# Kernel tuning notes

Measured on AMD Instinct MI355X. Metric: run time of the kernel, lower is better.

The kernel has to match this reference:

```python
import jax, jax.numpy as jnp
import numpy as np

T, B = 32, 64
D_IN = 512      # input_size == embedding dim
H = 512         # hidden_size
V = 32000       # n_vocab
F_FEAT = 768    # feature_size
NH = 8          # num_heads
HD = H // NH    # head_dim


def setup_inputs() -> dict:
    key = jax.random.key(0)
    ks = jax.random.split(key, 16)
    s = 0.02
    inp = {
        'y': jax.random.randint(ks[0], (T, B), 0, V),
        'ctx': jax.random.normal(ks[1], (1, B, F_FEAT), jnp.float32),
        'emb_W': jax.random.normal(ks[2], (V, D_IN), jnp.float32) * s,
        # GRUCell dec0: gates ordered (r, z, n) as in torch
        'W_ih': jax.random.normal(ks[3], (3 * H, D_IN), jnp.float32) * s,
        'b_ih': jnp.zeros((3 * H,), jnp.float32),
        'W_hh': jax.random.normal(ks[4], (3 * H, H), jnp.float32) * s,
        'b_hh': jnp.zeros((3 * H,), jnp.float32),
        # FF att: feature_size -> hidden, tanh
        'W_att': jax.random.normal(ks[5], (H, F_FEAT), jnp.float32) * s,
        'b_att': jnp.zeros((H,), jnp.float32),
        # MultiHeadSelfAttention projections (hidden -> hidden)
        'Wq': jax.random.normal(ks[6], (H, H), jnp.float32) * s,
        'bq': jnp.zeros((H,), jnp.float32),
        'Wk': jax.random.normal(ks[7], (H, H), jnp.float32) * s,
        'bk': jnp.zeros((H,), jnp.float32),
        'Wv': jax.random.normal(ks[8], (H, H), jnp.float32) * s,
        'bv': jnp.zeros((H,), jnp.float32),
        'Wfc': jax.random.normal(ks[9], (H, H), jnp.float32) * s,
        'bfc': jnp.zeros((H,), jnp.float32),
        # FF hid2out: hidden -> input, tanh, bias_zero
        'W_h2o': jax.random.normal(ks[10], (D_IN, H), jnp.float32) * s,
        'b_h2o': jnp.zeros((D_IN,), jnp.float32),
        # FF out2prob: input -> vocab, linear
        'W_out': jax.random.normal(ks[11], (V, D_IN), jnp.float32) * s,
        'b_out': jnp.zeros((V,), jnp.float32),
    }
    return inp


def reference(y, ctx, emb_W, W_ih, b_ih, W_hh, b_hh, W_att, b_att,
              Wq, bq, Wk, bk, Wv, bv, Wfc, bfc, W_h2o, b_h2o, W_out, b_out):
    y_emb = emb_W[y]                                   # [T, B, D_IN]
    # ct is constant across decode steps: tanh FF over pooled image feature
    ct = jnp.tanh(ctx[0] @ W_att.T + b_att)            # [B, H]
    h0 = jnp.zeros((y.shape[1], H), y_emb.dtype)       # dec_init 'zero'

    def step(h, y_t):
        # torch GRUCell (gate order r, z, n)
        gi = y_t @ W_ih.T + b_ih                       # [B, 3H]
        gh = h @ W_hh.T + b_hh                         # [B, 3H]
        gi_r, gi_z, gi_n = jnp.split(gi, 3, axis=-1)
        gh_r, gh_z, gh_n = jnp.split(gh, 3, axis=-1)
        r = jax.nn.sigmoid(gi_r + gh_r)
        z = jax.nn.sigmoid(gi_z + gh_z)
        n = jnp.tanh(gi_n + r * gh_n)
        h1 = (1.0 - z) * n + z * h                     # [B, H]

        x = h1 * ct                                    # [B, H]
        # MultiHeadSelfAttention on a single vector, heads act as sequence
        q = (x @ Wq.T + bq).reshape(-1, NH, HD)        # [B, NH, HD]
        k = (x @ Wk.T + bk).reshape(-1, NH, HD)
        v = (x @ Wv.T + bv).reshape(-1, NH, HD)
        scores = jnp.einsum('bhd,bgd->bhg', q, k) / HD  # note: /head_dim (not sqrt)
        attw = jax.nn.softmax(scores, axis=-1)
        att_out = jnp.einsum('bhg,bgd->bhd', attw, v).reshape(-1, H)
        h2 = att_out @ Wfc.T + bfc                     # [B, H] (fc_out, vocab_size==H)

        logit = jnp.tanh(h2 @ W_h2o.T + b_h2o)         # [B, D_IN]
        prob = jax.nn.softmax(logit @ W_out.T + b_out, axis=-1)  # [B, V]
        return h1, prob                                # f_next returns h1 as next state

    _, probs = jax.lax.scan(step, h0, y_emb)           # [T, B, V]
    return probs
```

## Files before the change

### kernel.cpp

```cpp
#include <hip/hip_runtime.h>
#include <hip/hip_bf16.h>
#include <math.h>

typedef __bf16 bf16_t;
typedef __bf16 bf16x8 __attribute__((ext_vector_type(8)));
typedef __bf16 bf16x4 __attribute__((ext_vector_type(4)));
typedef float  f32x4  __attribute__((ext_vector_type(4)));

#define T_STEPS 32
#define BATCH   64
#define DIN     512
#define HID     512
#define VOCAB   32000
#define FFEAT   768
#define ROWS    2048
#define G3      1536
#define NBLK_A  32

#define EPI_F32  0
#define EPI_BF16 1
#define EPI_TANH 2

#define GLOAD16(gp, lp) __builtin_amdgcn_global_load_lds( \
    (const __attribute__((address_space(1))) void*)(gp),  \
    (__attribute__((address_space(3))) void*)(lp), 16, 0, 0)

#define PHASEK(BUF, MH, KS, STAGE_STMT, GATE_STMT)                            \
  {                                                                           \
    bf16x8 af_[4], bf_[4];                                                    \
    _Pragma("unroll")                                                         \
    for (int m2 = 0; m2 < 4; ++m2) {                                          \
      const int row = wm * 64 + m2 * 16 + la;                                 \
      const int sl = ((KS) * 4 + lg) ^ (row & 7);                             \
      af_[m2] =                                                               \
          *(const bf16x8*)&lds[((BUF)*4 + (MH)) * 8192 + row * 64 + sl * 8];  \
    }                                                                         \
    _Pragma("unroll")                                                         \
    for (int nj = 0; nj < 4; ++nj) {                                          \
      const int row = wn * 32 + (nj & 1) * 16 + la;                           \
      const int sl = ((KS) * 4 + lg) ^ (row & 7);                             \
      bf_[nj] =                                                               \
          *(const bf16x8*)&lds[((BUF)*4 + 2 + (nj >> 1)) * 8192 + row * 64 + sl * 8];\
    }                                                                         \
    STAGE_STMT;                                                               \
    GATE_STMT;                                                                \
    __builtin_amdgcn_s_barrier();                                             \
    __builtin_amdgcn_s_setprio(1);                                            \
    _Pragma("unroll")                                                         \
    for (int m2 = 0; m2 < 4; ++m2)                                            \
      _Pragma("unroll")                                                       \
      for (int nj = 0; nj < 4; ++nj)                                          \
        acc[(MH)*4 + m2][nj] =                                                \
            __builtin_amdgcn_mfma_f32_16x16x32_bf16(                          \
                af_[m2], bf_[nj], acc[(MH)*4 + m2][nj], 0, 0, 0);             \
    __builtin_amdgcn_s_setprio(0);                                            \
    __builtin_amdgcn_s_barrier();                                             \
  }

template<int KD>
__global__ __launch_bounds__(512, 2) void gemm_v(
    const bf16_t* __restrict__ A, const bf16_t* __restrict__ B,
    const float* __restrict__ bias, bf16_t* __restrict__ ecache,
    float* __restrict__ partial, int M, int N, int NB)
{
  __shared__ bf16_t lds[2 * 4 * 8192];
  __shared__ float psum[256][4];
  const int tid = threadIdx.x;
  const int lane = tid & 63, wv = tid >> 6;
  const int wm = wv >> 2, wn = wv & 3;
  const int la = lane & 15, lg = lane >> 4;

  const int lin = blockIdx.x;
  const int mt = M >> 8;
  const int cpx = (NB * mt) >> 3;
  const int wg = (lin & 7) * cpx + (lin >> 3);
  const int bn = wg / mt, bm = wg - bn * mt;

  auto stageA = [&](int buf, int h, int kt) {
    const size_t base = (size_t)(bm * 256 + h * 128) * KD + (size_t)kt * 64;
#pragma unroll
    for (int q = 0; q < 2; ++q) {
      const int L = q * 512 + tid;
      const int row = L >> 3, sl = L & 7;
      const int c = sl ^ (row & 7);
      GLOAD16(A + base + (size_t)row * KD + c * 8,
              &lds[(buf * 4 + h) * 8192 + L * 8]);
    }
  };
  auto stageB = [&](int buf, int h, int kt) {
    const size_t base = (size_t)(bn * 256 + h * 128) * KD + (size_t)kt * 64;
#pragma unroll
    for (int q = 0; q < 2; ++q) {
      const int L = q * 512 + tid;
      const int row = L >> 3, sl = L & 7;
      const int c = sl ^ (row & 7);
      GLOAD16(B + base + (size_t)row * KD + c * 8,
              &lds[(buf * 4 + 2 + h) * 8192 + L * 8]);
    }
  };

  f32x4 acc[8][4] = {};
  constexpr int NITER = KD >> 7;

  stageA(0, 0, 0); stageA(0, 1, 0); stageB(0, 0, 0); stageB(0, 1, 0);
  stageA(1, 0, 1);
  asm volatile("s_waitcnt vmcnt(2)" ::: "memory");
  __builtin_amdgcn_s_barrier();

#pragma unroll
  for (int it = 0; it < NITER; ++it) {
    const int t0 = 2 * it;
    const bool lastI = (it == NITER - 1);
    PHASEK(0, 0, 0, { stageA(1, 1, t0 + 1); stageB(1, 0, t0 + 1); }, ;)
    PHASEK(0, 0, 1, { stageB(1, 1, t0 + 1); }, ;)
    PHASEK(0, 1, 0, { if (!lastI) stageA(0, 0, t0 + 2); }, ;)
    PHASEK(0, 1, 1, { },
           { if (lastI) { asm volatile("s_waitcnt vmcnt(0)" ::: "memory"); }
             else       { asm volatile("s_waitcnt vmcnt(2)" ::: "memory"); } })
    PHASEK(1, 0, 0, { if (!lastI) { stageA(0, 1, t0 + 2); stageB(0, 0, t0 + 2); } }, ;)
    PHASEK(1, 0, 1, { if (!lastI) stageB(0, 1, t0 + 2); }, ;)
    PHASEK(1, 1, 0, { if (!lastI) stageA(1, 0, t0 + 3); }, ;)
    PHASEK(1, 1, 1, { },
           { if (!lastI) { asm volatile("s_waitcnt vmcnt(2)" ::: "memory"); } })
  }

  float bv[4];
#pragma unroll
  for (int nj = 0; nj < 4; ++nj) {
    const int col = bn * 256 + (nj >> 1) * 128 + wn * 32 + (nj & 1) * 16 + la;
    bv[nj] = bias[col];
  }
  const int odd = la & 1;
#pragma unroll
  for (int mi = 0; mi < 8; ++mi) {
#pragma unroll
    for (int rr = 0; rr < 4; ++rr) {
      const int rowl = (mi >> 2) * 128 + wm * 64 + (mi & 3) * 16 + lg * 4 + rr;
      const int row = bm * 256 + rowl;
      float vsum = 0.f;
#pragma unroll
      for (int nj = 0; nj < 4; ++nj) {
        const float e = expf(acc[mi][nj][rr] + bv[nj]);
        vsum += e;
        const unsigned int mine =
            (unsigned int)__builtin_bit_cast(unsigned short, (bf16_t)e);
        const unsigned int other = (unsigned int)__shfl_xor((int)mine, 1);
        if (!odd) {
          const int col = bn * 256 + (nj >> 1) * 128 + wn * 32 + (nj & 1) * 16 + la;
          *(unsigned int*)&ecache[(size_t)row * N + col] = mine | (other << 16);
        }
      }
      vsum += __shfl_xor(vsum, 1);
      vsum += __shfl_xor(vsum, 2);
      vsum += __shfl_xor(vsum, 4);
      vsum += __shfl_xor(vsum, 8);
      if (la == 0) psum[rowl][wn] = vsum;
    }
  }
  __syncthreads();
  if (tid < 256) {
    partial[(size_t)(bm * 256 + tid) * NB + bn] =
        psum[tid][0] + psum[tid][1] + psum[tid][2] + psum[tid][3];
  }
}

template<int EPI, int KD>
__global__ __launch_bounds__(256) void gemm_lds(
    const bf16_t* __restrict__ A, const bf16_t* __restrict__ B,
    const float* __restrict__ bias, void* __restrict__ out, int M, int N)
{
  __shared__ bf16_t As[3][128 * 32];
  __shared__ bf16_t Bs[3][128 * 32];

  const int lane = threadIdx.x & 63;
  const int wv   = threadIdx.x >> 6;
  const int wm = wv >> 1, wn = wv & 1;
  const int bn = blockIdx.x, bm = blockIdx.y;
  const int la = lane & 15, lg = lane >> 4;
  const int tid = threadIdx.x;

  auto stage = [&](int buf, int k0) {
#pragma unroll
    for (int q = 0; q < 2; ++q) {
      const int idx = q * 256 + tid;
      const int row = idx >> 2, c = idx & 3;
      const int gch = c ^ ((row >> 1) & 3);
      GLOAD16(A + (size_t)(bm * 128 + row) * KD + k0 + gch * 8, &As[buf][idx * 8]);
      GLOAD16(B + (size_t)(bn * 128 + row) * KD + k0 + gch * 8, &Bs[buf][idx * 8]);
    }
  };
  const int rdch = (lg ^ ((la >> 1) & 3)) * 8;

  f32x4 acc[4][4] = {};
  constexpr int NT = KD >> 5;
  stage(0, 0);
  stage(1, 32);
  for (int kt = 0; kt < NT; ++kt) {
    if (kt + 1 < NT) {
      asm volatile("s_waitcnt vmcnt(4)" ::: "memory");
    } else {
      asm volatile("s_waitcnt vmcnt(0)" ::: "memory");
    }
    __builtin_amdgcn_s_barrier();
    __builtin_amdgcn_sched_barrier(0);
    if (kt + 2 < NT) stage((kt + 2) % 3, (kt + 2) * 32);
    const bf16_t* Ab = As[kt % 3];
    const bf16_t* Bb = Bs[kt % 3];
    bf16x8 a[4], b[4];
#pragma unroll
    for (int i = 0; i < 4; ++i)
      a[i] = *(const bf16x8*)(Ab + (wm * 64 + i * 16 + la) * 32 + rdch);
#pragma unroll
    for (int j = 0; j < 4; ++j)
      b[j] = *(const bf16x8*)(Bb + (wn * 64 + j * 16 + la) * 32 + rdch);
    __builtin_amdgcn_s_setprio(1);
#pragma unroll
    for (int i = 0; i < 4; ++i)
#pragma unroll
      for (int j = 0; j < 4; ++j)
        acc[i][j] = __builtin_amdgcn_mfma_f32_16x16x32_bf16(a[i], b[j], acc[i][j], 0, 0, 0);
    __builtin_amdgcn_s_setprio(0);
  }

  const int m0 = bm * 128 + wm * 64;
  const int n0 = bn * 128 + wn * 64;
  float bv4[4];
#pragma unroll
  for (int j = 0; j < 4; ++j) bv4[j] = bias[n0 + j * 16 + la];
#pragma unroll
  for (int i = 0; i < 4; ++i) {
#pragma unroll
    for (int r = 0; r < 4; ++r) {
      const int row = m0 + i * 16 + lg * 4 + r;
#pragma unroll
      for (int j = 0; j < 4; ++j) {
        const int col = n0 + j * 16 + la;
        float v = acc[i][j][r] + bv4[j];
        if constexpr (EPI == EPI_F32) {
          ((float*)out)[(size_t)row * N + col] = v;
        } else if constexpr (EPI == EPI_BF16) {
          ((bf16_t*)out)[(size_t)row * N + col] = (bf16_t)v;
        } else {
          ((bf16_t*)out)[(size_t)row * N + col] = (bf16_t)tanhf(v);
        }
      }
    }
  }
}

__global__ __launch_bounds__(256) void phaseA_k(
    const bf16_t* __restrict__ Wg, const float* __restrict__ bhh,
    const float* __restrict__ gi, const float* __restrict__ ct,
    unsigned int* __restrict__ hbuf, bf16_t* __restrict__ Xall,
    int* __restrict__ flags, const float* __restrict__ Wout_f32,
    bf16_t* __restrict__ WoutB)
{
  __shared__ bf16_t Wl[48 * 520];
  __shared__ float bl[48];
  const int tid = threadIdx.x, blk = blockIdx.x;

  if (blk >= NBLK_A) {
    const int NCB = gridDim.x - NBLK_A;
    const int n4 = VOCAB * DIN / 4;
    for (int i = (blk - NBLK_A) * 256 + tid; i < n4; i += NCB * 256) {
      float4 v = ((const float4*)Wout_f32)[i];
      bf16x4 o = {(bf16_t)v.x, (bf16_t)v.y, (bf16_t)v.z, (bf16_t)v.w};
      *(bf16x4*)(WoutB + (size_t)i * 4) = o;
    }
    return;
  }

  for (int i = tid; i < 48 * 64; i += 256) {
    const int rw = i >> 6, ch = (i & 63) << 3;
    *(bf16x8*)(Wl + rw * 520 + ch) = *(const bf16x8*)(Wg + (size_t)(blk * 48 + rw) * 512 + ch);
  }
  if (tid < 48) bl[tid] = bhh[blk * 48 + tid];
  __syncthreads();

  const int lane = tid & 63, wv = tid >> 6;
  const int la = lane & 15, lg = lane >> 4;
  const int jcol = blk * 16 + la;
  const int rowA = wv * 16 + la;

  const float blr = bl[la], blz = bl[16 + la], bln = bl[32 + la];
  float hprev[4], ctv[4];
#pragma unroll
  for (int r = 0; r < 4; ++r) {
    hprev[r] = 0.f;
    ctv[r] = ct[(size_t)(wv * 16 + lg * 4 + r) * HID + jcol];
  }

  for (int t = 0; t < T_STEPS; ++t) {
    const float* girow = gi + (size_t)t * BATCH * G3 + (size_t)blk * 48;
    float gv[12];
#pragma unroll
    for (int r = 0; r < 4; ++r) {
      const float* gp = girow + (size_t)(wv * 16 + lg * 4 + r) * G3;
      gv[r * 3 + 0] = gp[la];
      gv[r * 3 + 1] = gp[16 + la];
      gv[r * 3 + 2] = gp[32 + la];
    }
    if (t > 0) {
      if (lane < 32) {
        while (__hip_atomic_load(&flags[(lane * 4 + wv) * 16], __ATOMIC_RELAXED,
                                 __HIP_MEMORY_SCOPE_AGENT) < t) { }
      }
      asm volatile("" ::: "memory");
    }
    const unsigned long long* hb =
        (const unsigned long long*)(hbuf + (size_t)(t & 1) * 16384);
    bf16x8 af[16];
#pragma unroll
    for (int q = 0; q < 16; ++q) {
      union { unsigned long long u[2]; bf16x8 v; } c;
      const size_t bidx = (size_t)(2 * q + (lg >> 1)) * 256 + rowA * 4 + (lg & 1) * 2;
      c.u[0] = __hip_atomic_load(hb + bidx,     __ATOMIC_RELAXED, __HIP_MEMORY_SCOPE_AGENT);
      c.u[1] = __hip_atomic_load(hb + bidx + 1, __ATOMIC_RELAXED, __HIP_MEMORY_SCOPE_AGENT);
      af[q] = c.v;
    }
    f32x4 acc0 = {}, acc1 = {}, acc2 = {};
#pragma unroll
    for (int q = 0; q < 16; ++q) {
      const bf16_t* wp = Wl + q * 32 + lg * 8;
      bf16x8 b0 = *(const bf16x8*)(wp + (0 * 16 + la) * 520);
      bf16x8 b1 = *(const bf16x8*)(wp + (1 * 16 + la) * 520);
      bf16x8 b2 = *(const bf16x8*)(wp + (2 * 16 + la) * 520);
      acc0 = __builtin_amdgcn_mfma_f32_16x16x32_bf16(af[q], b0, acc0, 0, 0, 0);
      acc1 = __builtin_amdgcn_mfma_f32_16x16x32_bf16(af[q], b1, acc1, 0, 0, 0);
      acc2 = __builtin_amdgcn_mfma_f32_16x16x32_bf16(af[q], b2, acc2, 0, 0, 0);
    }
    float h1v[4];
#pragma unroll
    for (int r = 0; r < 4; ++r) {
      const float ghr = acc0[r] + blr;
      const float ghz = acc1[r] + blz;
      const float ghn = acc2[r] + bln;
      const float rr = 1.f / (1.f + expf(-(gv[r * 3 + 0] + ghr)));
      const float zz = 1.f / (1.f + expf(-(gv[r * 3 + 1] + ghz)));
      const float nn = tanhf(gv[r * 3 + 2] + rr * ghn);
      h1v[r] = (1.f - zz) * nn + zz * hprev[r];
      hprev[r] = h1v[r];
    }
    unsigned int* hn = hbuf + (size_t)((t + 1) & 1) * 16384 + blk * 512;
#pragma unroll
    for (int r = 0; r < 4; ++r) {
      const int row = wv * 16 + lg * 4 + r;
      const unsigned int mine =
          (unsigned int)__builtin_bit_cast(unsigned short, (bf16_t)h1v[r]);
      const unsigned int other = (unsigned int)__shfl_xor((int)mine, 1);
      if ((la & 1) == 0) {
        __hip_atomic_store(hn + row * 8 + (la >> 1), mine | (other << 16),
                           __ATOMIC_RELAXED, __HIP_MEMORY_SCOPE_AGENT);
      }
    }
    asm volatile("s_waitcnt vmcnt(0)" ::: "memory");
    if (lane == 0) {
      __hip_atomic_store(&flags[(blk * 4 + wv) * 16], t + 1, __ATOMIC_RELAXED,
                         __HIP_MEMORY_SCOPE_AGENT);
    }
#pragma unroll
    for (int r = 0; r < 4; ++r) {
      const int row = wv * 16 + lg * 4 + r;
      Xall[((size_t)t * BATCH + row) * HID + jcol] = (bf16_t)(h1v[r] * ctv[r]);
    }
  }
}

__global__ __launch_bounds__(256) void attn_k(const bf16_t* __restrict__ QKV,
                                              bf16_t* __restrict__ attO)
{
  __shared__ float sq[4][512], sk[4][512], sv[4][512], sw[4][64];
  const int tid = threadIdx.x;
  const int wv = tid >> 6, lane = tid & 63;
  const int row = blockIdx.x * 4 + wv;
  const bf16_t* base = QKV + (size_t)row * G3;
  bf16x8 vq = *(const bf16x8*)(base + lane * 8);
  bf16x8 vk = *(const bf16x8*)(base + 512 + lane * 8);
  bf16x8 vv = *(const bf16x8*)(base + 1024 + lane * 8);
#pragma unroll
  for (int e = 0; e < 8; ++e) {
    sq[wv][lane * 8 + e] = (float)vq[e];
    sk[wv][lane * 8 + e] = (float)vk[e];
    sv[wv][lane * 8 + e] = (float)vv[e];
  }
  __syncthreads();
  const int h = lane >> 3, g = lane & 7;
  float s = 0.f;
#pragma unroll 16
  for (int d = 0; d < 64; ++d) s += sq[wv][h * 64 + d] * sk[wv][g * 64 + d];
  s *= (1.f / 64.f);
  float m = s;
  m = fmaxf(m, __shfl_xor(m, 1));
  m = fmaxf(m, __shfl_xor(m, 2));
  m = fmaxf(m, __shfl_xor(m, 4));
  const float e = expf(s - m);
  float sum = e;
  sum += __shfl_xor(sum, 1);
  sum += __shfl_xor(sum, 2);
  sum += __shfl_xor(sum, 4);
  sw[wv][lane] = e / sum;
  __syncthreads();
#pragma unroll
  for (int rep = 0; rep < 8; ++rep) {
    const int idx = rep * 64 + lane;
    const int hh = idx >> 6, d = idx & 63;
    float o = 0.f;
#pragma unroll
    for (int gg = 0; gg < 8; ++gg) o += sw[wv][hh * 8 + gg] * sv[wv][gg * 64 + d];
    attO[(size_t)row * HID + idx] = (bf16_t)o;
  }
}

__global__ __launch_bounds__(256) void cast5_k(
    const float* __restrict__ s0, const float* __restrict__ s1,
    const float* __restrict__ s2, const float* __restrict__ s3,
    const float* __restrict__ s4, bf16_t* __restrict__ Wqkv,
    bf16_t* __restrict__ WfcB, bf16_t* __restrict__ Wh2oB)
{
  const int seg = blockIdx.x >> 8;
  const int i = (blockIdx.x & 255) * 256 + threadIdx.x;
  const float* src = seg == 0 ? s0 : seg == 1 ? s1 : seg == 2 ? s2
                   : seg == 3 ? s3 : s4;
  bf16_t* dst = seg <= 2 ? Wqkv + (size_t)seg * HID * DIN
              : seg == 3 ? WfcB : Wh2oB;
  float4 v = ((const float4*)src)[i];
  bf16x4 o = {(bf16_t)v.x, (bf16_t)v.y, (bf16_t)v.z, (bf16_t)v.w};
  *(bf16x4*)(dst + (size_t)i * 4) = o;
}

__global__ __launch_bounds__(256) void perm_cast_k(const float* __restrict__ src,
                                                   bf16_t* __restrict__ dst)
{
  const int i = blockIdx.x * 256 + threadIdx.x;
  const int pg = i >> 7, kq = (i & 127) << 2;
  const int g = pg / 48, rem = pg - g * 48, sec = rem >> 4, jj = rem & 15;
  const int srow = sec * 512 + g * 16 + jj;
  float4 v = *(const float4*)(src + (size_t)srow * DIN + kq);
  bf16x4 o = {(bf16_t)v.x, (bf16_t)v.y, (bf16_t)v.z, (bf16_t)v.w};
  *(bf16x4*)(dst + (size_t)pg * DIN + kq) = o;
}

__global__ void perm_bias_k(const float* __restrict__ bih, const float* __restrict__ bhh,
                            float* __restrict__ bihp, float* __restrict__ bhhp)
{
  const int pg = blockIdx.x * 256 + threadIdx.x;
  if (pg >= G3) return;
  const int g = pg / 48, rem = pg - g * 48, sec = rem >> 4, jj = rem & 15;
  const int srow = sec * 512 + g * 16 + jj;
  bihp[pg] = bih[srow];
  bhhp[pg] = bhh[srow];
}

__global__ void bcat_k(const float* __restrict__ a, const float* __restrict__ b,
                       const float* __restrict__ c, float* __restrict__ d)
{
  const int i = blockIdx.x * 256 + threadIdx.x;
  if (i >= G3) return;
  d[i] = i < 512 ? a[i] : (i < 1024 ? b[i - 512] : c[i - 1024]);
}

__global__ __launch_bounds__(256) void yemb_k(const int* __restrict__ y,
                                              const float* __restrict__ embW,
                                              bf16_t* __restrict__ out)
{
  const int idx = blockIdx.x * 256 + threadIdx.x;
  const int rb = idx >> 6, c = (idx & 63) << 3;
  const int tok = y[rb];
  const float4* s = (const float4*)(embW + (size_t)tok * DIN + c);
  float4 v0 = s[0], v1 = s[1];
  bf16x8 o = {(bf16_t)v0.x, (bf16_t)v0.y, (bf16_t)v0.z, (bf16_t)v0.w,
              (bf16_t)v1.x, (bf16_t)v1.y, (bf16_t)v1.z, (bf16_t)v1.w};
  *(bf16x8*)(out + (size_t)rb * DIN + c) = o;
}

__global__ __launch_bounds__(256) void ct_k(const float* __restrict__ ctx,
                                            const float* __restrict__ Watt,
                                            const float* __restrict__ batt,
                                            float* __restrict__ ct)
{
  const int idx = blockIdx.x * 256 + threadIdx.x;
  const int b = idx >> 9, j = idx & 511;
  const float4* c4 = (const float4*)(ctx + (size_t)b * FFEAT);
  const float4* w4 = (const float4*)(Watt + (size_t)j * FFEAT);
  float s = batt[j];
  for (int q = 0; q < FFEAT / 4; ++q) {
    float4 cc = c4[q], ww = w4[q];
    s += cc.x * ww.x + cc.y * ww.y + cc.z * ww.z + cc.w * ww.w;
  }
  ct[idx] = tanhf(s);
}

__global__ __launch_bounds__(256) void reduce_rows(const float* __restrict__ partial,
                                                   float* __restrict__ rowsum, int NB)
{
  const int wv = threadIdx.x >> 6, lane = threadIdx.x & 63;
  const int row = blockIdx.x * 4 + wv;
  float s = 0.f;
  for (int c = lane; c < NB; c += 64) s += partial[(size_t)row * NB + c];
  for (int m = 1; m < 64; m <<= 1) s += __shfl_xor(s, m);
  if (lane == 0) rowsum[row] = s;
}

__global__ __launch_bounds__(256) void normalize_k(const bf16_t* __restrict__ e,
                                                   const float* __restrict__ rowsum,
                                                   float* __restrict__ out)
{
  const int row = blockIdx.y;
  const int c8 = blockIdx.x * 256 + threadIdx.x;
  if (c8 >= VOCAB / 8) return;
  const float inv = 1.0f / rowsum[row];
  const size_t base = (size_t)row * VOCAB + (size_t)c8 * 8;
  bf16x8 v = *(const bf16x8*)(e + base);
  float4 o0 = {(float)v[0] * inv, (float)v[1] * inv, (float)v[2] * inv, (float)v[3] * inv};
  float4 o1 = {(float)v[4] * inv, (float)v[5] * inv, (float)v[6] * inv, (float)v[7] * inv};
  *(float4*)(out + base) = o0;
  *(float4*)(out + base + 4) = o1;
}

extern "C" void kernel_launch(void* const* d_in, const int* in_sizes, int n_in,
                              void* d_out, int out_size, void* d_ws, size_t ws_size,
                              hipStream_t stream)
{
  const int*   y     = (const int*)  d_in[0];
  const float* ctx   = (const float*)d_in[1];
  const float* embW  = (const float*)d_in[2];
  const float* W_ih  = (const float*)d_in[3];
  const float* b_ih  = (const float*)d_in[4];
  const float* W_hh  = (const float*)d_in[5];
  const float* b_hh  = (const float*)d_in[6];
  const float* W_att = (const float*)d_in[7];
  const float* b_att = (const float*)d_in[8];
  const float* Wq    = (const float*)d_in[9];
  const float* bq    = (const float*)d_in[10];
  const float* Wk    = (const float*)d_in[11];
  const float* bk    = (const float*)d_in[12];
  const float* Wv    = (const float*)d_in[13];
  const float* bv    = (const float*)d_in[14];
  const float* Wfc   = (const float*)d_in[15];
  const float* bfc   = (const float*)d_in[16];
  const float* Wh2o  = (const float*)d_in[17];
  const float* bh2o  = (const float*)d_in[18];
  const float* W_out = (const float*)d_in[19];
  const float* b_out = (const float*)d_in[20];

  char* p = (char*)d_ws;
  auto alloc = [&](size_t bytes) {
    char* r = p;
    p += (bytes + 255) & ~(size_t)255;
    return r;
  };
  bf16_t* WoutB   = (bf16_t*)alloc((size_t)VOCAB * DIN * 2);
  bf16_t* WgIh    = (bf16_t*)alloc((size_t)G3 * DIN * 2);
  bf16_t* WgHh    = (bf16_t*)alloc((size_t)G3 * DIN * 2);
  bf16_t* Wqkv    = (bf16_t*)alloc((size_t)G3 * DIN * 2);
  bf16_t* WfcB    = (bf16_t*)alloc((size_t)HID * HID * 2);
  bf16_t* Wh2oB   = (bf16_t*)alloc((size_t)HID * HID * 2);
  float*  bIhP    = (float*)alloc(G3 * 4);
  float*  bHhP    = (float*)alloc(G3 * 4);
  float*  bQkv    = (float*)alloc(G3 * 4);
  bf16_t* Yemb    = (bf16_t*)alloc((size_t)ROWS * DIN * 2);
  float*  giP     = (float*)alloc((size_t)ROWS * G3 * 4);
  float*  ctB     = (float*)alloc((size_t)BATCH * HID * 4);
  unsigned int* hbuf = (unsigned int*)alloc((size_t)2 * 16384 * 4);
  bf16_t* Xall    = (bf16_t*)alloc((size_t)ROWS * DIN * 2);
  bf16_t* QKV     = (bf16_t*)alloc((size_t)ROWS * G3 * 2);
  bf16_t* attO    = (bf16_t*)alloc((size_t)ROWS * HID * 2);
  bf16_t* h2B     = (bf16_t*)alloc((size_t)ROWS * HID * 2);
  bf16_t* logit   = (bf16_t*)alloc((size_t)ROWS * DIN * 2);
  float*  partial = (float*)alloc((size_t)ROWS * 125 * 4);
  float*  rowsum  = (float*)alloc((size_t)ROWS * 4);
  int*    flags   = (int*)alloc(32 * 4 * 64);
  bf16_t* eCache  = (bf16_t*)alloc((size_t)ROWS * VOCAB * 2);

  hipMemsetAsync(hbuf, 0, (size_t)2 * 16384 * 4, stream);
  hipMemsetAsync(flags, 0, 32 * 4 * 64, stream);

  cast5_k<<<1280, 256, 0, stream>>>(Wq, Wk, Wv, Wfc, Wh2o, Wqkv, WfcB, Wh2oB);
  perm_cast_k<<<768, 256, 0, stream>>>(W_ih, WgIh);
  perm_cast_k<<<768, 256, 0, stream>>>(W_hh, WgHh);
  perm_bias_k<<<6, 256, 0, stream>>>(b_ih, b_hh, bIhP, bHhP);
  bcat_k<<<6, 256, 0, stream>>>(bq, bk, bv, bQkv);
  yemb_k<<<512, 256, 0, stream>>>(y, embW, Yemb);
  ct_k<<<128, 256, 0, stream>>>(ctx, W_att, b_att, ctB);

  gemm_lds<EPI_F32, DIN><<<dim3(12, 16), 256, 0, stream>>>(
      Yemb, WgIh, bIhP, giP, ROWS, G3);

  phaseA_k<<<224, 256, 0, stream>>>(WgHh, bHhP, giP, ctB, hbuf, Xall, flags,
                                    W_out, WoutB);

  gemm_lds<EPI_BF16, DIN><<<dim3(12, 16), 256, 0, stream>>>(
      Xall, Wqkv, bQkv, QKV, ROWS, G3);

  attn_k<<<512, 256, 0, stream>>>(QKV, attO);

  gemm_lds<EPI_BF16, HID><<<dim3(4, 16), 256, 0, stream>>>(
      attO, WfcB, bfc, h2B, ROWS, HID);

  gemm_lds<EPI_TANH, HID><<<dim3(4, 16), 256, 0, stream>>>(
      h2B, Wh2oB, bh2o, logit, ROWS, DIN);

  gemm_v<DIN><<<1000, 512, 0, stream>>>(
      logit, WoutB, b_out, eCache, partial, ROWS, VOCAB, 125);
  reduce_rows<<<512, 256, 0, stream>>>(partial, rowsum, 125);
  normalize_k<<<dim3(16, ROWS), 256, 0, stream>>>(eCache, rowsum, (float*)d_out);
}
```

Measured before the change: 455.4 us.

## Fuse input-gate GEMM and weight casts into recurrent kernel; rework vocab GEMM pipeline

The separate input-projection GEMM (Yemb x W_ih) and its fp32 gi buffer are removed. The recurrent GRU kernel now computes the input gates itself with extra MFMAs per step from an LDS-resident W_ih slice. The Q/K/V/fc/h2o weight casts are folded into the idle cast blocks of that kernel, dropping one launch. Separately, the large vocab GEMM's pipeline is restructured from fine-grained per-phase barriers to a simpler double-buffered scheme with fewer barriers. This trades extra per-step compute on the serial recurrence critical path for fewer launches and less memory traffic.

```diff
diff --git a/kernel.cpp b/kernel.cpp
--- a/kernel.cpp
+++ b/kernel.cpp
@@ -16,6 +16,7 @@
 #define ROWS    2048
 #define G3      1536
 #define NBLK_A  32
+#define NBLK_CC 192
 
 #define EPI_F32  0
 #define EPI_BF16 1
@@ -25,7 +26,7 @@
     (const __attribute__((address_space(1))) void*)(gp),  \
     (__attribute__((address_space(3))) void*)(lp), 16, 0, 0)
 
-#define PHASEK(BUF, MH, KS, STAGE_STMT, GATE_STMT)                            \
+#define PHASEQ(BUF, MH, KS)                                                   \
   {                                                                           \
     bf16x8 af_[4], bf_[4];                                                    \
     _Pragma("unroll")                                                         \
@@ -42,9 +43,6 @@
       bf_[nj] =                                                               \
           *(const bf16x8*)&lds[((BUF)*4 + 2 + (nj >> 1)) * 8192 + row * 64 + sl * 8];\
     }                                                                         \
-    STAGE_STMT;                                                               \
-    GATE_STMT;                                                                \
-    __builtin_amdgcn_s_barrier();                                             \
     __builtin_amdgcn_s_setprio(1);                                            \
     _Pragma("unroll")                                                         \
     for (int m2 = 0; m2 < 4; ++m2)                                            \
@@ -54,7 +52,6 @@
             __builtin_amdgcn_mfma_f32_16x16x32_bf16(                          \
                 af_[m2], bf_[nj], acc[(MH)*4 + m2][nj], 0, 0, 0);             \
     __builtin_amdgcn_s_setprio(0);                                            \
-    __builtin_amdgcn_s_barrier();                                             \
   }
 
 template<int KD>
@@ -100,28 +97,33 @@
   };
 
   f32x4 acc[8][4] = {};
-  constexpr int NITER = KD >> 7;
+  constexpr int NT = KD >> 6;
 
   stageA(0, 0, 0); stageA(0, 1, 0); stageB(0, 0, 0); stageB(0, 1, 0);
-  stageA(1, 0, 1);
-  asm volatile("s_waitcnt vmcnt(2)" ::: "memory");
-  __builtin_amdgcn_s_barrier();
-
-#pragma unroll
-  for (int it = 0; it < NITER; ++it) {
-    const int t0 = 2 * it;
-    const bool lastI = (it == NITER - 1);
-    PHASEK(0, 0, 0, { stageA(1, 1, t0 + 1); stageB(1, 0, t0 + 1); }, ;)
-    PHASEK(0, 0, 1, { stageB(1, 1, t0 + 1); }, ;)
-    PHASEK(0, 1, 0, { if (!lastI) stageA(0, 0, t0 + 2); }, ;)
-    PHASEK(0, 1, 1, { },
-           { if (lastI) { asm volatile("s_waitcnt vmcnt(0)" ::: "memory"); }
-             else       { asm volatile("s_waitcnt vmcnt(2)" ::: "memory"); } })
-    PHASEK(1, 0, 0, { if (!lastI) { stageA(0, 1, t0 + 2); stageB(0, 0, t0 + 2); } }, ;)
-    PHASEK(1, 0, 1, { if (!lastI) stageB(0, 1, t0 + 2); }, ;)
-    PHASEK(1, 1, 0, { if (!lastI) stageA(1, 0, t0 + 3); }, ;)
-    PHASEK(1, 1, 1, { },
-           { if (!lastI) { asm volatile("s_waitcnt vmcnt(2)" ::: "memory"); } })
+  stageA(1, 0, 1); stageA(1, 1, 1); stageB(1, 0, 1); stageB(1, 1, 1);
+
+#pragma unroll
+  for (int kt = 0; kt < NT; ++kt) {
+    const int buf = kt & 1;
+    if (kt == 0) {
+      asm volatile("s_waitcnt vmcnt(8)" ::: "memory");
+    } else if (kt == NT - 1) {
+      asm volatile("s_waitcnt vmcnt(0)" ::: "memory");
+    } else {
+      asm volatile("s_waitcnt vmcnt(2)" ::: "memory");
+    }
+    __builtin_amdgcn_s_barrier();
+    if (kt > 0 && kt + 1 < NT) {
+      stageA(buf ^ 1, 1, kt + 1);
+      stageB(buf ^ 1, 0, kt + 1);
+      stageB(buf ^ 1, 1, kt + 1);
+    }
+    PHASEQ(buf, 0, 0)
+    PHASEQ(buf, 0, 1)
+    __builtin_amdgcn_s_barrier();
+    if (kt + 2 < NT) stageA(buf, 0, kt + 2);
+    PHASEQ(buf, 1, 0)
+    PHASEQ(buf, 1, 1)
   }
 
   float bv[4];
@@ -249,32 +251,55 @@
 }
 
 __global__ __launch_bounds__(256) void phaseA_k(
-    const bf16_t* __restrict__ Wg, const float* __restrict__ bhh,
-    const float* __restrict__ gi, const float* __restrict__ ct,
-    unsigned int* __restrict__ hbuf, bf16_t* __restrict__ Xall,
-    int* __restrict__ flags, const float* __restrict__ Wout_f32,
-    bf16_t* __restrict__ WoutB)
-{
-  __shared__ bf16_t Wl[48 * 520];
-  __shared__ float bl[48];
+    const bf16_t* __restrict__ WgIh, const bf16_t* __restrict__ WgHh,
+    const float* __restrict__ bihp, const float* __restrict__ bhhp,
+    const float* __restrict__ ct, unsigned int* __restrict__ hbuf,
+    bf16_t* __restrict__ Xall, int* __restrict__ flags,
+    const bf16_t* __restrict__ Yemb,
+    const float* __restrict__ Wout_f32, bf16_t* __restrict__ WoutB,
+    const float* __restrict__ Wq, const float* __restrict__ Wk,
+    const float* __restrict__ Wv, const float* __restrict__ Wfc,
+    const float* __restrict__ Wh2o, bf16_t* __restrict__ Wqkv,
+    bf16_t* __restrict__ WfcB, bf16_t* __restrict__ Wh2oB)
+{
+  __shared__ bf16_t Wih[48 * 520];
+  __shared__ bf16_t Whh[48 * 520];
+  __shared__ float bl[96];
   const int tid = threadIdx.x, blk = blockIdx.x;
 
   if (blk >= NBLK_A) {
-    const int NCB = gridDim.x - NBLK_A;
+    const int s = blk - NBLK_A;
     const int n4 = VOCAB * DIN / 4;
-    for (int i = (blk - NBLK_A) * 256 + tid; i < n4; i += NCB * 256) {
+    for (int i = s * 256 + tid; i < n4; i += NBLK_CC * 256) {
       float4 v = ((const float4*)Wout_f32)[i];
       bf16x4 o = {(bf16_t)v.x, (bf16_t)v.y, (bf16_t)v.z, (bf16_t)v.w};
       *(bf16x4*)(WoutB + (size_t)i * 4) = o;
     }
+    const int m4 = HID * HID / 4;
+    for (int i = s * 256 + tid; i < 5 * m4; i += NBLK_CC * 256) {
+      const int seg = i >> 16, j = i & (m4 - 1);
+      const float* src = seg == 0 ? Wq : seg == 1 ? Wk : seg == 2 ? Wv
+                       : seg == 3 ? Wfc : Wh2o;
+      bf16_t* dst = seg <= 2 ? Wqkv + (size_t)seg * HID * DIN
+                  : seg == 3 ? WfcB : Wh2oB;
+      float4 v = ((const float4*)src)[j];
+      bf16x4 o = {(bf16_t)v.x, (bf16_t)v.y, (bf16_t)v.z, (bf16_t)v.w};
+      *(bf16x4*)(dst + (size_t)j * 4) = o;
+    }
     return;
   }
 
   for (int i = tid; i < 48 * 64; i += 256) {
     const int rw = i >> 6, ch = (i & 63) << 3;
-    *(bf16x8*)(Wl + rw * 520 + ch) = *(const bf16x8*)(Wg + (size_t)(blk * 48 + rw) * 512 + ch);
-  }
-  if (tid < 48) bl[tid] = bhh[blk * 48 + tid];
+    *(bf16x8*)(Wih + rw * 520 + ch) =
+        *(const bf16x8*)(WgIh + (size_t)(blk * 48 + rw) * 512 + ch);
+    *(bf16x8*)(Whh + rw * 520 + ch) =
+        *(const bf16x8*)(WgHh + (size_t)(blk * 48 + rw) * 512 + ch);
+  }
+  if (tid < 48) {
+    bl[tid] = bihp[blk * 48 + tid];
+    bl[48 + tid] = bhhp[blk * 48 + tid];
+  }
   __syncthreads();
 
   const int lane = tid & 63, wv = tid >> 6;
@@ -282,7 +307,8 @@
   const int jcol = blk * 16 + la;
   const int rowA = wv * 16 + la;
 
-  const float blr = bl[la], blz = bl[16 + la], bln = bl[32 + la];
+  const float br_i = bl[la],      bz_i = bl[16 + la], bn_i = bl[32 + la];
+  const float br_h = bl[48 + la], bz_h = bl[64 + la], bn_h = bl[80 + la];
   float hprev[4], ctv[4];
 #pragma unroll
   for (int r = 0; r < 4; ++r) {
@@ -291,15 +317,10 @@
   }
 
   for (int t = 0; t < T_STEPS; ++t) {
-    const float* girow = gi + (size_t)t * BATCH * G3 + (size_t)blk * 48;
-    float gv[12];
-#pragma unroll
-    for (int r = 0; r < 4; ++r) {
-      const float* gp = girow + (size_t)(wv * 16 + lg * 4 + r) * G3;
-      gv[r * 3 + 0] = gp[la];
-      gv[r * 3 + 1] = gp[16 + la];
-      gv[r * 3 + 2] = gp[32 + la];
-    }
+    const bf16_t* yrow = Yemb + ((size_t)t * BATCH + rowA) * DIN + lg * 8;
+    bf16x8 ay[16];
+#pragma unroll
+    for (int q = 0; q < 16; ++q) ay[q] = *(const bf16x8*)(yrow + q * 32);
     if (t > 0) {
       if (lane < 32) {
         while (__hip_atomic_load(&flags[(lane * 4 + wv) * 16], __ATOMIC_RELAXED,
@@ -309,35 +330,33 @@
     }
     const unsigned long long* hb =
         (const unsigned long long*)(hbuf + (size_t)(t & 1) * 16384);
-    bf16x8 af[16];
+    bf16x8 ah[16];
 #pragma unroll
     for (int q = 0; q < 16; ++q) {
       union { unsigned long long u[2]; bf16x8 v; } c;
       const size_t bidx = (size_t)(2 * q + (lg >> 1)) * 256 + rowA * 4 + (lg & 1) * 2;
       c.u[0] = __hip_atomic_load(hb + bidx,     __ATOMIC_RELAXED, __HIP_MEMORY_SCOPE_AGENT);
       c.u[1] = __hip_atomic_load(hb + bidx + 1, __ATOMIC_RELAXED, __HIP_MEMORY_SCOPE_AGENT);
-      af[q] = c.v;
-    }
-    f32x4 acc0 = {}, acc1 = {}, acc2 = {};
+      ah[q] = c.v;
+    }
+    f32x4 ry = {}, zy = {}, ny = {}, rh = {}, zh = {}, nh = {};
 #pragma unroll
     for (int q = 0; q < 16; ++q) {
-      const bf16_t* wp = Wl + q * 32 + lg * 8;
-      bf16x8 b0 = *(const bf16x8*)(wp + (0 * 16 + la) * 520);
-      bf16x8 b1 = *(const bf16x8*)(wp + (1 * 16 + la) * 520);
-      bf16x8 b2 = *(const bf16x8*)(wp + (2 * 16 + la) * 520);
-      acc0 = __builtin_amdgcn_mfma_f32_16x16x32_bf16(af[q], b0, acc0, 0, 0, 0);
-      acc1 = __builtin_amdgcn_mfma_f32_16x16x32_bf16(af[q], b1, acc1, 0, 0, 0);
-      acc2 = __builtin_amdgcn_mfma_f32_16x16x32_bf16(af[q], b2, acc2, 0, 0, 0);
+      const bf16_t* wi = Wih + q * 32 + lg * 8;
+      const bf16_t* wh = Whh + q * 32 + lg * 8;
+      ry = __builtin_amdgcn_mfma_f32_16x16x32_bf16(ay[q], *(const bf16x8*)(wi + (la) * 520), ry, 0, 0, 0);
+      zy = __builtin_amdgcn_mfma_f32_16x16x32_bf16(ay[q], *(const bf16x8*)(wi + (16 + la) * 520), zy, 0, 0, 0);
+      ny = __builtin_amdgcn_mfma_f32_16x16x32_bf16(ay[q], *(const bf16x8*)(wi + (32 + la) * 520), ny, 0, 0, 0);
+      rh = __builtin_amdgcn_mfma_f32_16x16x32_bf16(ah[q], *(const bf16x8*)(wh + (la) * 520), rh, 0, 0, 0);
+      zh = __builtin_amdgcn_mfma_f32_16x16x32_bf16(ah[q], *(const bf16x8*)(wh + (16 + la) * 520), zh, 0, 0, 0);
+      nh = __builtin_amdgcn_mfma_f32_16x16x32_bf16(ah[q], *(const bf16x8*)(wh + (32 + la) * 520), nh, 0, 0, 0);
     }
     float h1v[4];
 #pragma unroll
     for (int r = 0; r < 4; ++r) {
-      const float ghr = acc0[r] + blr;
-      const float ghz = acc1[r] + blz;
-      const float ghn = acc2[r] + bln;
-      const float rr = 1.f / (1.f + expf(-(gv[r * 3 + 0] + ghr)));
-      const float zz = 1.f / (1.f + expf(-(gv[r * 3 + 1] + ghz)));
-      const float nn = tanhf(gv[r * 3 + 2] + rr * ghn);
+      const float rr = 1.f / (1.f + expf(-(ry[r] + rh[r] + br_i + br_h)));
+      const float zz = 1.f / (1.f + expf(-(zy[r] + zh[r] + bz_i + bz_h)));
+      const float nn = tanhf((ny[r] + bn_i) + rr * (nh[r] + bn_h));
       h1v[r] = (1.f - zz) * nn + zz * hprev[r];
       hprev[r] = h1v[r];
     }
@@ -409,23 +428,6 @@
     for (int gg = 0; gg < 8; ++gg) o += sw[wv][hh * 8 + gg] * sv[wv][gg * 64 + d];
     attO[(size_t)row * HID + idx] = (bf16_t)o;
   }
-}
-
-__global__ __launch_bounds__(256) void cast5_k(
-    const float* __restrict__ s0, const float* __restrict__ s1,
-    const float* __restrict__ s2, const float* __restrict__ s3,
-    const float* __restrict__ s4, bf16_t* __restrict__ Wqkv,
-    bf16_t* __restrict__ WfcB, bf16_t* __restrict__ Wh2oB)
-{
-  const int seg = blockIdx.x >> 8;
-  const int i = (blockIdx.x & 255) * 256 + threadIdx.x;
-  const float* src = seg == 0 ? s0 : seg == 1 ? s1 : seg == 2 ? s2
-                   : seg == 3 ? s3 : s4;
-  bf16_t* dst = seg <= 2 ? Wqkv + (size_t)seg * HID * DIN
-              : seg == 3 ? WfcB : Wh2oB;
-  float4 v = ((const float4*)src)[i];
-  bf16x4 o = {(bf16_t)v.x, (bf16_t)v.y, (bf16_t)v.z, (bf16_t)v.w};
-  *(bf16x4*)(dst + (size_t)i * 4) = o;
 }
 
 __global__ __launch_bounds__(256) void perm_cast_k(const float* __restrict__ src,
@@ -559,7 +561,6 @@
   float*  bHhP    = (float*)alloc(G3 * 4);
   float*  bQkv    = (float*)alloc(G3 * 4);
   bf16_t* Yemb    = (bf16_t*)alloc((size_t)ROWS * DIN * 2);
-  float*  giP     = (float*)alloc((size_t)ROWS * G3 * 4);
   float*  ctB     = (float*)alloc((size_t)BATCH * HID * 4);
   unsigned int* hbuf = (unsigned int*)alloc((size_t)2 * 16384 * 4);
   bf16_t* Xall    = (bf16_t*)alloc((size_t)ROWS * DIN * 2);
@@ -569,13 +570,12 @@
   bf16_t* logit   = (bf16_t*)alloc((size_t)ROWS * DIN * 2);
   float*  partial = (float*)alloc((size_t)ROWS * 125 * 4);
   float*  rowsum  = (float*)alloc((size_t)ROWS * 4);
-  int*    flags   = (int*)alloc(32 * 4 * 64);
+  int*    flags   = (int*)alloc(16384);
   bf16_t* eCache  = (bf16_t*)alloc((size_t)ROWS * VOCAB * 2);
 
   hipMemsetAsync(hbuf, 0, (size_t)2 * 16384 * 4, stream);
-  hipMemsetAsync(flags, 0, 32 * 4 * 64, stream);
-
-  cast5_k<<<1280, 256, 0, stream>>>(Wq, Wk, Wv, Wfc, Wh2o, Wqkv, WfcB, Wh2oB);
+  hipMemsetAsync(flags, 0, 16384, stream);
+
   perm_cast_k<<<768, 256, 0, stream>>>(W_ih, WgIh);
   perm_cast_k<<<768, 256, 0, stream>>>(W_hh, WgHh);
   perm_bias_k<<<6, 256, 0, stream>>>(b_ih, b_hh, bIhP, bHhP);
@@ -583,11 +583,9 @@
   yemb_k<<<512, 256, 0, stream>>>(y, embW, Yemb);
   ct_k<<<128, 256, 0, stream>>>(ctx, W_att, b_att, ctB);
 
-  gemm_lds<EPI_F32, DIN><<<dim3(12, 16), 256, 0, stream>>>(
-      Yemb, WgIh, bIhP, giP, ROWS, G3);
-
-  phaseA_k<<<224, 256, 0, stream>>>(WgHh, bHhP, giP, ctB, hbuf, Xall, flags,
-                                    W_out, WoutB);
+  phaseA_k<<<NBLK_A + NBLK_CC, 256, 0, stream>>>(
+      WgIh, WgHh, bIhP, bHhP, ctB, hbuf, Xall, flags, Yemb,
+      W_out, WoutB, Wq, Wk, Wv, Wfc, Wh2o, Wqkv, WfcB, Wh2oB);
 
   gemm_lds<EPI_BF16, DIN><<<dim3(12, 16), 256, 0, stream>>>(
       Xall, Wqkv, bQkv, QKV, ROWS, G3);
```

After: 478.7 us. 5.1% more time.
